# Performance work log

Measured on AMD Instinct MI355X. Metric: run time of the kernel, lower is better.

The kernel has to match this reference:

```python
import jax, jax.numpy as jnp
import numpy as np

MARGIN = 0.3


def setup_inputs() -> dict:
    key = jax.random.key(0)
    k1, k2 = jax.random.split(key)
    N, D, C = 8192, 512, 1024
    embeddings = jax.random.normal(k1, (N, D), dtype=jnp.float32)
    labels = jax.random.randint(k2, (N,), 0, C, dtype=jnp.int64)
    return {"embeddings": embeddings, "labels": labels}


def reference(embeddings, labels):
    # L2-normalize rows, cosine distance via Gram matrix: d = 1 - e_i . e_j
    e = embeddings / jnp.linalg.norm(embeddings, axis=1, keepdims=True)
    dist = 1.0 - jnp.matmul(e, e.T)  # [N, N]

    same = labels[:, None] == labels[None, :]           # [N, N] bool
    eye = jnp.eye(labels.shape[0], dtype=bool)
    pos_mask = same & ~eye                              # positives exclude self
    neg_mask = ~same                                    # negatives

    # Batch-hard mining: hardest (farthest) positive, hardest (closest) negative
    hardest_pos = jnp.max(jnp.where(pos_mask, dist, -jnp.inf), axis=1)
    hardest_neg = jnp.min(jnp.where(neg_mask, dist, jnp.inf), axis=1)

    loss = jax.nn.relu(hardest_pos - hardest_neg + MARGIN)
    return jnp.mean(loss)
```

## Files before the change

kernel.cpp:

```cpp
#include <hip/hip_runtime.h>
#include <hip/hip_fp8.h>
#include <hip/hip_fp16.h>
#include <stdint.h>

#define MARGIN 0.3f

constexpr int N = 8192;
constexpr int D = 512;
constexpr int BM = 128, BN = 128;
constexpr int NKS = D / 64;
constexpr int NT = N / BM;
constexpr int NPAIR = NT * (NT + 1) / 2;
constexpr int WEDGE = NPAIR / 8;
constexpr float ESCALE = 16.0f;
constexpr float INV_SC2 = 1.0f / (ESCALE * ESCALE);

typedef int i32x8 __attribute__((ext_vector_type(8)));
typedef float f32x16 __attribute__((ext_vector_type(16)));
typedef __fp16 h2 __attribute__((ext_vector_type(2)));

constexpr unsigned INF2 = 0x7C007C00u;

__device__ __forceinline__ unsigned char f2fp8(float f) {
  return __hip_fp8_e4m3(f).__x;
}

__device__ __forceinline__ unsigned pkmin(unsigned a, unsigned b) {
  unsigned d;
  asm("v_pk_min_f16 %0, %1, %2" : "=v"(d) : "v"(a), "v"(b));
  return d;
}

__device__ __forceinline__ unsigned cvtpk(float lo, float hi) {
  union { h2 h; unsigned u; } cv;
  cv.h = __builtin_amdgcn_cvt_pkrtz(lo, hi);
  return cv.u;
}

__device__ __forceinline__ void pair_from_q(int q, int& ti, int& tj) {
  int SI = 0;
  while (32 * (SI + 1) * (SI + 1) + 4 * (SI + 1) <= q) ++SI;
  int r = q - (32 * SI * SI + 4 * SI);
  int i, j, SJ;
  if (r < 64 * SI) {
    SJ = r >> 6;
    int w = r & 63;
    i = w >> 3;
    j = w & 7;
  } else {
    int d = r - 64 * SI;
    SJ = SI;
    i = 0;
    while ((i + 1) * (i + 2) / 2 <= d) ++i;
    j = d - i * (i + 1) / 2;
  }
  ti = SI * 8 + i;
  tj = SJ * 8 + j;
}


__global__ __launch_bounds__(256) void normalize_rows(
    const float* __restrict__ emb, unsigned char* __restrict__ e8,
    float* __restrict__ out) {
  if (blockIdx.x == 0 && threadIdx.x == 0) out[0] = 0.f;
  const int wave = threadIdx.x >> 6, lane = threadIdx.x & 63;
  const int row = blockIdx.x * 4 + wave;
  const float4* src = (const float4*)(emb + (size_t)row * D);
  float4 x0 = src[lane];
  float4 x1 = src[lane + 64];
  float ss = x0.x * x0.x + x0.y * x0.y + x0.z * x0.z + x0.w * x0.w +
             x1.x * x1.x + x1.y * x1.y + x1.z * x1.z + x1.w * x1.w;
#pragma unroll
  for (int m = 1; m < 64; m <<= 1) ss += __shfl_xor(ss, m, 64);
  const float r = rsqrtf(ss) * ESCALE;
  union { unsigned char b[8]; uint2 u; } o;
  o.b[0] = f2fp8(x0.x * r); o.b[1] = f2fp8(x0.y * r);
  o.b[2] = f2fp8(x0.z * r); o.b[3] = f2fp8(x0.w * r);
  o.b[4] = f2fp8(x1.x * r); o.b[5] = f2fp8(x1.y * r);
  o.b[6] = f2fp8(x1.z * r); o.b[7] = f2fp8(x1.w * r);
  const int n = row & 31;
  const unsigned inner =
      ((unsigned)(n * 64 + ((lane >> 1) & 3) * 16) ^
       ((unsigned)((n >> 1) & 7) << 4)) + (lane & 1) * 8;
  const unsigned off = (unsigned)((row >> 5) * 8 + (lane >> 3)) * 2048 + inner;
  *(uint2*)(e8 + off) = o.u;
}

__global__ __launch_bounds__(256, 3) void bh_gemm_sym(
    const unsigned char* __restrict__ e8, const int* __restrict__ labels,
    unsigned* __restrict__ scr) {
  __shared__ unsigned char lds[2][16384];
  __shared__ unsigned bufR[2][128];
  __shared__ unsigned bufC[2][128];

  const int b = blockIdx.x;
  const int q = WEDGE * (b & 7) + (b >> 3);
  int ti, tj;
  pair_from_q(q, ti, tj);
  const int iBase = ti * BM, jBase = tj * BN;
  const bool diag = (ti == tj);

  const int tid = threadIdx.x;
  const int lane = tid & 63;
  const int wave = tid >> 6;
  const int wr = wave >> 1, wc = wave & 1;
  const int n = lane & 31, hi = lane >> 5;

  const unsigned o0 =
      (unsigned)(n * 64 + hi * 32) ^ ((unsigned)((n >> 1) & 7) << 4);

  const unsigned char* gsrc[4];
  unsigned ldst[4];
#pragma unroll
  for (int j = 0; j < 4; ++j) {
    const int id = wave * 4 + j;
    const int mat = id >> 3;
    const int fb = (id & 7) >> 1;
    const int rb = (mat ? (jBase >> 5) : (iBase >> 5)) + fb;
    gsrc[j] = e8 + (size_t)(rb * 8) * 2048 + (id & 1) * 1024 + lane * 16;
    ldst[j] = (unsigned)id * 1024 + lane * 16;
  }

  auto STAGE = [&](int T, int buf) {
#pragma unroll
    for (int j = 0; j < 4; ++j)
      __builtin_amdgcn_global_load_lds(
          (const __attribute__((address_space(1))) unsigned int*)(gsrc[j] +
                                                                  (size_t)T * 2048),
          (__attribute__((address_space(3))) unsigned int*)(&lds[buf][ldst[j]]),
          16, 0, 0);
  };

  f32x16 acc[2][2];
#pragma unroll
  for (int t = 0; t < 2; ++t)
#pragma unroll
    for (int c = 0; c < 2; ++c) acc[t][c] = (f32x16)0.0f;

  STAGE(0, 0);
  __syncthreads();
#pragma unroll
  for (int T = 0; T < NKS; ++T) {
    const int cur = T & 1;
    if (T + 1 < NKS) STAGE(T + 1, cur ^ 1);
    union { i32x8 v; int4 q2[2]; } aF[2], bF[2];
#pragma unroll
    for (int t = 0; t < 2; ++t) {
      const unsigned char* ab = &lds[cur][(wr * 2 + t) * 2048];
      aF[t].q2[0] = *(const int4*)(ab + o0);
      aF[t].q2[1] = *(const int4*)(ab + (o0 ^ 16));
      const unsigned char* bb = &lds[cur][8192 + (wc * 2 + t) * 2048];
      bF[t].q2[0] = *(const int4*)(bb + o0);
      bF[t].q2[1] = *(const int4*)(bb + (o0 ^ 16));
    }
#pragma unroll
    for (int t = 0; t < 2; ++t)
#pragma unroll
      for (int c = 0; c < 2; ++c)
        acc[t][c] = __builtin_amdgcn_mfma_scale_f32_32x32x64_f8f6f4(
            aF[t].v, bF[c].v, acc[t][c], 0, 0,
            0, 127, 0, 127);
    __syncthreads();
  }

  int lj[2];
#pragma unroll
  for (int c = 0; c < 2; ++c) lj[c] = labels[jBase + wc * 64 + c * 32 + n];

  unsigned colAcc[2] = {INF2, INF2};

#pragma unroll
  for (int t = 0; t < 2; ++t) {
    int li[16];
#pragma unroll
    for (int a = 0; a < 4; ++a) {
      int4 v = *(const int4*)(labels + iBase + wr * 64 + t * 32 + 4 * hi + 8 * a);
      li[4 * a + 0] = v.x; li[4 * a + 1] = v.y;
      li[4 * a + 2] = v.z; li[4 * a + 3] = v.w;
    }
    unsigned P[2][16];
#pragma unroll
    for (int c = 0; c < 2; ++c) {
#pragma unroll
      for (int r = 0; r < 16; ++r) {
        const float s = acc[t][c][r];
        const unsigned u = cvtpk(s, -s);
        const bool same = (li[r] == lj[c]);
        const unsigned sel = same ? 0x0000FFFFu : 0xFFFF0000u;
        unsigned p = (sel & u) | (~sel & INF2);
        if (diag) {
          const int row32 = (r & 3) + 8 * (r >> 2) + 4 * hi;
          const bool self =
              (wr * 64 + t * 32 + row32) == (wc * 64 + c * 32 + n);
          p = self ? INF2 : p;
        }
        P[c][r] = p;
      }
      if (!diag) {
        unsigned cm = P[c][0];
#pragma unroll
        for (int r = 1; r < 16; ++r) cm = pkmin(cm, P[c][r]);
        colAcc[c] = pkmin(colAcc[c], cm);
      }
    }
    unsigned m[16];
#pragma unroll
    for (int r = 0; r < 16; ++r) m[r] = pkmin(P[0][r], P[1][r]);
    unsigned w8[8];
#pragma unroll
    for (int i = 0; i < 8; ++i) {
      unsigned x = pkmin(m[2 * i],     __shfl_xor(m[2 * i],     16, 64));
      unsigned y = pkmin(m[2 * i + 1], __shfl_xor(m[2 * i + 1], 16, 64));
      w8[i] = (lane & 16) ? y : x;
    }
    unsigned w4[4];
#pragma unroll
    for (int i = 0; i < 4; ++i) {
      unsigned x = pkmin(w8[2 * i],     __shfl_xor(w8[2 * i],     8, 64));
      unsigned y = pkmin(w8[2 * i + 1], __shfl_xor(w8[2 * i + 1], 8, 64));
      w4[i] = (lane & 8) ? y : x;
    }
    unsigned w2[2];
#pragma unroll
    for (int i = 0; i < 2; ++i) {
      unsigned x = pkmin(w4[2 * i],     __shfl_xor(w4[2 * i],     4, 64));
      unsigned y = pkmin(w4[2 * i + 1], __shfl_xor(w4[2 * i + 1], 4, 64));
      w2[i] = (lane & 4) ? y : x;
    }
    unsigned x1 = pkmin(w2[0], __shfl_xor(w2[0], 2, 64));
    unsigned y1 = pkmin(w2[1], __shfl_xor(w2[1], 2, 64));
    unsigned w1 = (lane & 2) ? y1 : x1;
    w1 = pkmin(w1, __shfl_xor(w1, 1, 64));
    const int row32 = 16 * ((lane >> 1) & 1) + 8 * ((lane >> 2) & 1) + 4 * hi +
                      2 * ((lane >> 3) & 1) + ((lane >> 4) & 1);
    if ((lane & 1) == 0) bufR[wc][wr * 64 + t * 32 + row32] = w1;
  }

  if (!diag) {
#pragma unroll
    for (int c = 0; c < 2; ++c)
      colAcc[c] = pkmin(colAcc[c], __shfl_xor(colAcc[c], 32, 64));
    if (hi == 0) {
#pragma unroll
      for (int c = 0; c < 2; ++c)
        bufC[wr][wc * 64 + c * 32 + n] = colAcc[c];
    }
  }

  __syncthreads();

  if (wc == 0) {
    const int row = wr * 64 + lane;
    scr[(unsigned)(iBase + row) * 64 + tj] = pkmin(bufR[0][row], bufR[1][row]);
  }
  if (!diag && wr == 0) {
    const int col = wc * 64 + lane;
    scr[(unsigned)(jBase + col) * 64 + ti] = pkmin(bufC[0][col], bufC[1][col]);
  }
}

__global__ __launch_bounds__(256) void finalize_loss(
    const unsigned* __restrict__ scr, float* __restrict__ out) {
  const int row = blockIdx.x * 256 + threadIdx.x;
  const uint4* p = (const uint4*)(scr + (size_t)row * 64);
  unsigned mm = INF2;
#pragma unroll
  for (int i = 0; i < 16; ++i) {
    uint4 w = p[i];
    mm = pkmin(mm, pkmin(pkmin(w.x, w.y), pkmin(w.z, w.w)));
  }
  const float mn = __half2float(__ushort_as_half((unsigned short)(mm & 0xffff)));
  const float nmx = __half2float(__ushort_as_half((unsigned short)(mm >> 16)));
  float loss = (-nmx - mn) * INV_SC2 + MARGIN;
  float sum = loss > 0.f ? loss : 0.f;
#pragma unroll
  for (int m = 1; m < 64; m <<= 1) sum += __shfl_xor(sum, m, 64);
  __shared__ float ws4[4];
  const int lane = threadIdx.x & 63, wave = threadIdx.x >> 6;
  if (lane == 0) ws4[wave] = sum;
  __syncthreads();
  if (threadIdx.x == 0)
    atomicAdd(out, (ws4[0] + ws4[1] + ws4[2] + ws4[3]) * (1.0f / N));
}

extern "C" void kernel_launch(void* const* d_in, const int* in_sizes, int n_in,
                              void* d_out, int out_size, void* d_ws, size_t ws_size,
                              hipStream_t stream) {
  const float* emb = (const float*)d_in[0];
  const int* labels = (const int*)d_in[1];
  float* out = (float*)d_out;

  unsigned char* e8 = (unsigned char*)d_ws;
  unsigned* scr = (unsigned*)((char*)d_ws + (size_t)4 * 1024 * 1024);

  normalize_rows<<<N / 4, 256, 0, stream>>>(emb, e8, out);
  bh_gemm_sym<<<NPAIR, 256, 0, stream>>>(e8, labels, scr);
  finalize_loss<<<N / 256, 256, 0, stream>>>(scr, out);
}
```

Before: 102.6 us.

## Load MFMA fragments directly from global memory, dropping LDS staging

The normalize kernel now writes the fp8 embeddings in an order that matches the MFMA fragment layout, so each lane's 32-byte fragment is contiguous in global memory. The GEMM kernel drops the LDS double buffer and its barriers. Each wave instead loads its fragments straight from global memory into registers, prefetching two k-steps ahead. This removes LDS traffic and synchronisation, but the waves no longer share tiles, so global/L2 traffic goes up and register pressure grows.

```diff
diff --git a/kernel.cpp b/kernel.cpp
--- a/kernel.cpp
+++ b/kernel.cpp
@@ -80,8 +80,7 @@
   o.b[6] = f2fp8(x1.z * r); o.b[7] = f2fp8(x1.w * r);
   const int n = row & 31;
   const unsigned inner =
-      ((unsigned)(n * 64 + ((lane >> 1) & 3) * 16) ^
-       ((unsigned)((n >> 1) & 7) << 4)) + (lane & 1) * 8;
+      (unsigned)(n * 32) + ((unsigned)((lane >> 2) & 1)) * 1024 + (lane & 3) * 8;
   const unsigned off = (unsigned)((row >> 5) * 8 + (lane >> 3)) * 2048 + inner;
   *(uint2*)(e8 + off) = o.u;
 }
@@ -89,7 +88,6 @@
 __global__ __launch_bounds__(256, 3) void bh_gemm_sym(
     const unsigned char* __restrict__ e8, const int* __restrict__ labels,
     unsigned* __restrict__ scr) {
-  __shared__ unsigned char lds[2][16384];
   __shared__ unsigned bufR[2][128];
   __shared__ unsigned bufC[2][128];
 
@@ -106,30 +104,30 @@
   const int wr = wave >> 1, wc = wave & 1;
   const int n = lane & 31, hi = lane >> 5;
 
-  const unsigned o0 =
-      (unsigned)(n * 64 + hi * 32) ^ ((unsigned)((n >> 1) & 7) << 4);
-
-  const unsigned char* gsrc[4];
-  unsigned ldst[4];
-#pragma unroll
-  for (int j = 0; j < 4; ++j) {
-    const int id = wave * 4 + j;
-    const int mat = id >> 3;
-    const int fb = (id & 7) >> 1;
-    const int rb = (mat ? (jBase >> 5) : (iBase >> 5)) + fb;
-    gsrc[j] = e8 + (size_t)(rb * 8) * 2048 + (id & 1) * 1024 + lane * 16;
-    ldst[j] = (unsigned)id * 1024 + lane * 16;
-  }
-
-  auto STAGE = [&](int T, int buf) {
-#pragma unroll
-    for (int j = 0; j < 4; ++j)
-      __builtin_amdgcn_global_load_lds(
-          (const __attribute__((address_space(1))) unsigned int*)(gsrc[j] +
-                                                                  (size_t)T * 2048),
-          (__attribute__((address_space(3))) unsigned int*)(&lds[buf][ldst[j]]),
-          16, 0, 0);
-  };
+  const unsigned char* pA0 =
+      e8 + (size_t)(ti * 4 + wr * 2 + 0) * 16384 + lane * 32;
+  const unsigned char* pA1 =
+      e8 + (size_t)(ti * 4 + wr * 2 + 1) * 16384 + lane * 32;
+  const unsigned char* pB0 =
+      e8 + (size_t)(tj * 4 + wc * 2 + 0) * 16384 + lane * 32;
+  const unsigned char* pB1 =
+      e8 + (size_t)(tj * 4 + wc * 2 + 1) * 16384 + lane * 32;
+
+  union Frag { i32x8 v; int4 q2[2]; };
+  Frag pa[2][2], pb[2][2];
+
+#define PREF(ph)                                       \
+  {                                                    \
+    pa[ph][0].q2[0] = *(const int4*)(pA0);             \
+    pa[ph][0].q2[1] = *(const int4*)(pA0 + 16);        \
+    pa[ph][1].q2[0] = *(const int4*)(pA1);             \
+    pa[ph][1].q2[1] = *(const int4*)(pA1 + 16);        \
+    pb[ph][0].q2[0] = *(const int4*)(pB0);             \
+    pb[ph][0].q2[1] = *(const int4*)(pB0 + 16);        \
+    pb[ph][1].q2[0] = *(const int4*)(pB1);             \
+    pb[ph][1].q2[1] = *(const int4*)(pB1 + 16);        \
+    pA0 += 2048; pA1 += 2048; pB0 += 2048; pB1 += 2048; \
+  }
 
   f32x16 acc[2][2];
 #pragma unroll
@@ -137,31 +135,21 @@
 #pragma unroll
     for (int c = 0; c < 2; ++c) acc[t][c] = (f32x16)0.0f;
 
-  STAGE(0, 0);
-  __syncthreads();
+  PREF(0);
+  PREF(1);
 #pragma unroll
   for (int T = 0; T < NKS; ++T) {
-    const int cur = T & 1;
-    if (T + 1 < NKS) STAGE(T + 1, cur ^ 1);
-    union { i32x8 v; int4 q2[2]; } aF[2], bF[2];
-#pragma unroll
-    for (int t = 0; t < 2; ++t) {
-      const unsigned char* ab = &lds[cur][(wr * 2 + t) * 2048];
-      aF[t].q2[0] = *(const int4*)(ab + o0);
-      aF[t].q2[1] = *(const int4*)(ab + (o0 ^ 16));
-      const unsigned char* bb = &lds[cur][8192 + (wc * 2 + t) * 2048];
-      bF[t].q2[0] = *(const int4*)(bb + o0);
-      bF[t].q2[1] = *(const int4*)(bb + (o0 ^ 16));
-    }
+    const int ph = T & 1;
 #pragma unroll
     for (int t = 0; t < 2; ++t)
 #pragma unroll
       for (int c = 0; c < 2; ++c)
         acc[t][c] = __builtin_amdgcn_mfma_scale_f32_32x32x64_f8f6f4(
-            aF[t].v, bF[c].v, acc[t][c], 0, 0,
+            pa[ph][t].v, pb[ph][c].v, acc[t][c], 0, 0,
             0, 127, 0, 127);
-    __syncthreads();
-  }
+    if (T + 2 < NKS) PREF(ph);
+  }
+#undef PREF
 
   int lj[2];
 #pragma unroll
```

New measurement: 105.9 us. 3.2% more time.
